# Kernel optimization log

Measured on AMD Instinct MI355X. Metric: run time of the kernel, lower is better.

## Reference

```python
import jax, jax.numpy as jnp
import numpy as np

VOCAB, D, SLOTS, K = 50257, 512, 16, 3
B, T_FULL = 64, 2049
EPS_LN = 1e-5


def setup_inputs() -> dict:
    key = jax.random.key(0)
    ks = jax.random.split(key, 12)
    u = jax.random.uniform(ks[0], (B, T_FULL - 1), jnp.float32)
    gumbel = -jnp.log(-jnp.log(u + 1e-8) + 1e-8)
    s = 0.02
    return {
        "seq": jax.random.randint(ks[1], (B, T_FULL), 0, VOCAB),
        "temperature": jnp.ones((), jnp.float32),
        "gumbel": gumbel,
        "embed": jax.random.normal(ks[2], (VOCAB, D), jnp.float32) * s,
        "W1": jax.random.normal(ks[3], (D, 2 * D), jnp.float32) * s,
        "b1": jnp.zeros((2 * D,), jnp.float32),
        "W2": jax.random.normal(ks[4], (2 * D, D), jnp.float32) * s,
        "b2": jnp.zeros((D,), jnp.float32),
        "gamma": jnp.ones((D,), jnp.float32),
        "beta": jnp.zeros((D,), jnp.float32),
        "Wg": jax.random.normal(ks[5], (D,), jnp.float32) * s,
        "bg": jnp.zeros((), jnp.float32),
        "Wr": jax.random.normal(ks[6], (D, D), jnp.float32) * s,
        "br": jnp.zeros((D,), jnp.float32),
        "Wo": jax.random.normal(ks[7], (D, VOCAB), jnp.float32) * s,
        "bo": jnp.zeros((VOCAB,), jnp.float32),
    }


def reference(seq, temperature, gumbel, embed, W1, b1, W2, b2, gamma, beta, Wg, bg, Wr, br, Wo, bo):
    # Encoder: embed -> FFN residual -> LayerNorm
    h = embed[seq]                                        # [B, T+1, D]
    ff = jnp.maximum(h @ W1 + b1, 0.0) @ W2 + b2
    x = h + ff
    mu = jnp.mean(x, -1, keepdims=True)
    var = jnp.mean((x - mu) ** 2, -1, keepdims=True)
    hiddens = (x - mu) * jax.lax.rsqrt(var + EPS_LN) * gamma + beta

    context = hiddens[:, :-1, :]                          # [B, T, D]
    gate = context @ Wg + bg                              # [B, T]

    # gumbel top-k with straight-through mask (forward value = hard mask)
    perturbed = (gate + gumbel) / temperature
    _, idx = jax.lax.top_k(perturbed, K)                  # [B, K]
    mask = jnp.zeros_like(gate).at[jnp.arange(B)[:, None], idx].set(1.0)
    soft = jax.nn.softmax(perturbed, axis=-1)
    sel = mask + soft - jax.lax.stop_gradient(soft)

    # gather selected hidden states, scatter_add into memory slots
    gw = jnp.take_along_axis(sel, idx, axis=1)            # [B, K]
    gh = jnp.take_along_axis(context, idx[..., None], axis=1)  # [B, K, D]
    weighted = gh * gw[..., None]
    slot_idx = jnp.arange(K) % SLOTS
    mem = jnp.zeros((B, SLOTS, D), hiddens.dtype).at[:, slot_idx, :].add(weighted)

    # attention read with last-position query
    q = hiddens[:, -1, :] @ Wr + br                       # [B, D]
    scores = jnp.einsum('bsd,bd->bs', mem, q)
    attn = jax.nn.softmax(scores, axis=-1)
    ctx = jnp.einsum('bs,bsd->bd', attn, mem)
    return ctx @ Wo + bo                                  # [B, vocab]
```

## Files before the change

kernel.cpp:

```cpp
#include <hip/hip_runtime.h>
#include <math.h>

#define TFULL 2049
#define TCTX  2048
#define Vm    50257

typedef __attribute__((ext_vector_type(8))) short bf16x8;
typedef __attribute__((ext_vector_type(4))) short s16x4;
typedef __attribute__((ext_vector_type(4))) float f32x4;

__device__ __forceinline__ float wred64(float v){
  #pragma unroll
  for (int m = 1; m < 64; m <<= 1) v += __shfl_xor(v, m, 64);
  return v;
}
__device__ __forceinline__ short bf16_rn(float x){
  union { float f; unsigned u; } c; c.f = x;
  unsigned r = c.u + 0x7fff + ((c.u >> 16) & 1);
  return (short)(r >> 16);
}
__device__ __forceinline__ float bf16_f(short s){
  union { float f; unsigned u; } c; c.u = ((unsigned)(unsigned short)s) << 16;
  return c.f;
}

#define FMA4(ACC_, S_, W_)                         \
  (ACC_).x = fmaf((S_), (W_).x, (ACC_).x);         \
  (ACC_).y = fmaf((S_), (W_).y, (ACC_).y);         \
  (ACC_).z = fmaf((S_), (W_).z, (ACC_).z);         \
  (ACC_).w = fmaf((S_), (W_).w, (ACC_).w);

__global__ void k0_setup(const float* __restrict__ gamma, const float* __restrict__ beta,
                         const float* __restrict__ Wg, float* __restrict__ scal){
  const int t = threadIdx.x;
  float wg = Wg[t];
  float g  = gamma[t]*wg, bw = beta[t]*wg;
  scal[2 + t] = g;
  g = wred64(g); bw = wred64(bw);
  __shared__ float ra[8], rb[8];
  if ((t & 63) == 0){ ra[t>>6] = g; rb[t>>6] = bw; }
  __syncthreads();
  if (t == 0){
    float G = 0.f, Bw = 0.f;
    #pragma unroll
    for (int i = 0; i < 8; ++i){ G += ra[i]; Bw += rb[i]; }
    scal[0] = G; scal[1] = Bw;
  }
}

__global__ __launch_bounds__(256) void kpack(const float* __restrict__ W, int N, int KB,
                                             short* __restrict__ hi, short* __restrict__ lo){
  int i = blockIdx.x*256 + threadIdx.x;
  if (i >= KB*N*4) return;
  int kq = i & 3;
  int n  = (i >> 2) % N;
  int kb = i / (N*4);
  const float* src = W + (kb*32 + kq*8)*N + n;
  bf16x8 h8, l8;
  #pragma unroll
  for (int j = 0; j < 8; ++j){
    float w = src[j*N];
    short h = bf16_rn(w);
    h8[j] = h;
    l8[j] = bf16_rn(w - bf16_f(h));
  }
  *(bf16x8*)(hi + i*8) = h8;
  *(bf16x8*)(lo + i*8) = l8;
}

__global__ __launch_bounds__(512, 2) void k1_main(
    const int*   __restrict__ seq,   const float* __restrict__ temp,
    const float* __restrict__ gumbel,const float* __restrict__ embed,
    const short* __restrict__ W1h,   const short* __restrict__ W1l,
    const float* __restrict__ b1,
    const short* __restrict__ W2h,   const short* __restrict__ W2l,
    const float* __restrict__ b2,
    const float* __restrict__ gamma, const float* __restrict__ beta,
    const float* __restrict__ bg,
    const float* __restrict__ scal,
    float* __restrict__ pert, float* __restrict__ qh)
{
  __shared__ short Ah[8*2048];
  __shared__ short Al[8*2048];
  __shared__ short Rbuf[32768];
  __shared__ float Xq[512];
  __shared__ int   srow[64];
  __shared__ float redS1[512], redS2[512], redSG[512];
  __shared__ float redMu[64], redRs[64];

  short* Rh = Rbuf;
  short* Rl = Rbuf + 16384;

  const int t    = threadIdx.x;
  const int tile = blockIdx.x;
  const int lane = t & 63;
  const int wv   = t >> 6;
  const int mrow = lane & 15;
  const int kq   = lane >> 4;
  const int crow0 = kq*4;

  if (t < 64) srow[t] = seq[tile*64 + t];
  __syncthreads();

  const f32x4* __restrict__ embv = (const f32x4*)embed;

  auto stageA = [&](int hh){
    #pragma unroll
    for (int k = 0; k < 8; ++k){
      int idx = k*512 + t;
      int tok = idx >> 6, c4 = idx & 63;
      f32x4 v = embv[srow[tok]*128 + hh*64 + c4];
      int dl = c4*4;
      int base = (dl>>5)*2048 + ((dl>>3)&3)*512 + tok*8 + (dl&7);
      short h0 = bf16_rn(v[0]), h1 = bf16_rn(v[1]), h2 = bf16_rn(v[2]), h3 = bf16_rn(v[3]);
      *(s16x4*)(Ah + base) = (s16x4){h0, h1, h2, h3};
      *(s16x4*)(Al + base) = (s16x4){ bf16_rn(v[0] - bf16_f(h0)),
                                      bf16_rn(v[1] - bf16_f(h1)),
                                      bf16_rn(v[2] - bf16_f(h2)),
                                      bf16_rn(v[3] - bf16_f(h3)) };
    }
  };

  f32x4 ff[4][4];
  #pragma unroll
  for (int i = 0; i < 4; ++i)
    #pragma unroll
    for (int j = 0; j < 4; ++j) ff[i][j] = (f32x4){0.f,0.f,0.f,0.f};

  const int aoff = kq*512 + mrow*8;
  int boff2[4];
  #pragma unroll
  for (int nt = 0; nt < 4; ++nt)
    boff2[nt] = (wv*64 + nt*16 + mrow)*32 + kq*8;

  #pragma unroll 1
  for (int ch = 0; ch < 4; ++ch){
    f32x4 acc[2][4];
    #pragma unroll
    for (int i = 0; i < 2; ++i)
      #pragma unroll
      for (int j = 0; j < 4; ++j) acc[i][j] = (f32x4){0.f,0.f,0.f,0.f};

    int boff1[2];
    #pragma unroll
    for (int nt = 0; nt < 2; ++nt)
      boff1[nt] = (ch*256 + wv*32 + nt*16 + mrow)*32 + kq*8;

    auto g1 = [&](int hh){
      const short* whB = W1h + hh*262144;
      const short* wlB = W1l + hh*262144;
      bf16x8 ah[2][4], al[2][4], bh[2][2], bl[2][2];
      #pragma unroll
      for (int mt = 0; mt < 4; ++mt){
        ah[0][mt] = *(const bf16x8*)(Ah + aoff + mt*128);
        al[0][mt] = *(const bf16x8*)(Al + aoff + mt*128);
      }
      #pragma unroll
      for (int nt = 0; nt < 2; ++nt){
        bh[0][nt] = *(const bf16x8*)(whB + boff1[nt]);
        bl[0][nt] = *(const bf16x8*)(wlB + boff1[nt]);
      }
      #pragma unroll
      for (int kbr = 0; kbr < 8; ++kbr){
        const int cur = kbr & 1, nxt = cur ^ 1;
        if (kbr < 7){
          #pragma unroll
          for (int mt = 0; mt < 4; ++mt){
            ah[nxt][mt] = *(const bf16x8*)(Ah + (kbr+1)*2048 + aoff + mt*128);
            al[nxt][mt] = *(const bf16x8*)(Al + (kbr+1)*2048 + aoff + mt*128);
          }
          #pragma unroll
          for (int nt = 0; nt < 2; ++nt){
            bh[nxt][nt] = *(const bf16x8*)(whB + (kbr+1)*32768 + boff1[nt]);
            bl[nxt][nt] = *(const bf16x8*)(wlB + (kbr+1)*32768 + boff1[nt]);
          }
        }
        #pragma unroll
        for (int nt = 0; nt < 2; ++nt)
          #pragma unroll
          for (int mt = 0; mt < 4; ++mt){
            acc[nt][mt] = __builtin_amdgcn_mfma_f32_16x16x32_bf16(ah[cur][mt], bh[cur][nt], acc[nt][mt], 0,0,0);
            acc[nt][mt] = __builtin_amdgcn_mfma_f32_16x16x32_bf16(al[cur][mt], bh[cur][nt], acc[nt][mt], 0,0,0);
            acc[nt][mt] = __builtin_amdgcn_mfma_f32_16x16x32_bf16(ah[cur][mt], bl[cur][nt], acc[nt][mt], 0,0,0);
          }
      }
    };

    stageA(0);
    __syncthreads();
    g1(0);
    __syncthreads();
    stageA(1);
    __syncthreads();
    g1(1);
    __syncthreads();

    #pragma unroll
    for (int nt = 0; nt < 2; ++nt){
      int jcol = wv*32 + nt*16 + mrow;
      float bb = b1[ch*256 + jcol];
      int rbase = (jcol>>5)*2048 + ((jcol>>3)&3)*512 + (jcol&7);
      #pragma unroll
      for (int mt = 0; mt < 4; ++mt){
        #pragma unroll
        for (int r = 0; r < 4; ++r){
          int tok = mt*16 + crow0 + r;
          float a = fmaxf(acc[nt][mt][r] + bb, 0.f);
          short h = bf16_rn(a);
          Rh[rbase + tok*8] = h;
          Rl[rbase + tok*8] = bf16_rn(a - bf16_f(h));
        }
      }
    }
    __syncthreads();

    {
      const short* w2hB = W2h + ch*131072;
      const short* w2lB = W2l + ch*131072;
      bf16x8 rh2[2][4], rl2[2][4], bh2[2][4], bl2[2][4];
      #pragma unroll
      for (int mt = 0; mt < 4; ++mt){
        rh2[0][mt] = *(const bf16x8*)(Rh + aoff + mt*128);
        rl2[0][mt] = *(const bf16x8*)(Rl + aoff + mt*128);
      }
      #pragma unroll
      for (int nt = 0; nt < 4; ++nt){
        bh2[0][nt] = *(const bf16x8*)(w2hB + boff2[nt]);
        bl2[0][nt] = *(const bf16x8*)(w2lB + boff2[nt]);
      }
      #pragma unroll
      for (int kb = 0; kb < 8; ++kb){
        const int cur = kb & 1, nxt = cur ^ 1;
        if (kb < 7){
          #pragma unroll
          for (int mt = 0; mt < 4; ++mt){
            rh2[nxt][mt] = *(const bf16x8*)(Rh + (kb+1)*2048 + aoff + mt*128);
            rl2[nxt][mt] = *(const bf16x8*)(Rl + (kb+1)*2048 + aoff + mt*128);
          }
          #pragma unroll
          for (int nt = 0; nt < 4; ++nt){
            bh2[nxt][nt] = *(const bf16x8*)(w2hB + (kb+1)*16384 + boff2[nt]);
            bl2[nxt][nt] = *(const bf16x8*)(w2lB + (kb+1)*16384 + boff2[nt]);
          }
        }
        #pragma unroll
        for (int nt = 0; nt < 4; ++nt)
          #pragma unroll
          for (int mt = 0; mt < 4; ++mt){
            ff[nt][mt] = __builtin_amdgcn_mfma_f32_16x16x32_bf16(rh2[cur][mt], bh2[cur][nt], ff[nt][mt], 0,0,0);
            ff[nt][mt] = __builtin_amdgcn_mfma_f32_16x16x32_bf16(rl2[cur][mt], bh2[cur][nt], ff[nt][mt], 0,0,0);
            ff[nt][mt] = __builtin_amdgcn_mfma_f32_16x16x32_bf16(rh2[cur][mt], bl2[cur][nt], ff[nt][mt], 0,0,0);
          }
      }
    }
  }

  __syncthreads();
  float* hbuf = (float*)Rbuf;
  #pragma unroll
  for (int k = 0; k < 8; ++k){
    int idx = k*512 + t;
    int tok = idx >> 6, c4 = idx & 63;
    f32x4 v = embv[srow[tok]*128 + c4];
    f32x4 hv;
    #pragma unroll
    for (int j = 0; j < 4; ++j){
      short hi = bf16_rn(v[j]);
      hv[j] = bf16_f(hi) + bf16_f(bf16_rn(v[j] - bf16_f(hi)));
    }
    *(f32x4*)(hbuf + tok*256 + c4*4) = hv;
  }
  __syncthreads();

  const float G1 = scal[0], BW = scal[1];
  const float* gWg = scal + 2;
  const float bgv  = bg[0];
  const float invT = 1.0f / temp[0];
  int rem  = (tile*64) % 2049;
  int qtok = 2048 - rem;

  float ps1[4][4], ps2[4][4], psg[4][4];
  #pragma unroll
  for (int mt = 0; mt < 4; ++mt)
    #pragma unroll
    for (int r = 0; r < 4; ++r){ ps1[mt][r]=0.f; ps2[mt][r]=0.f; psg[mt][r]=0.f; }

  #pragma unroll
  for (int nt = 0; nt < 4; ++nt){
    int d = wv*64 + nt*16 + mrow;
    float b2v = b2[d];
    float gw  = gWg[d];
    if (wv >= 4){
      int abase = ((d - 256)>>5)*2048 + ((d>>3)&3)*512 + (d&7);
      #pragma unroll
      for (int mt = 0; mt < 4; ++mt){
        #pragma unroll
        for (int r = 0; r < 4; ++r){
          int tok = mt*16 + crow0 + r;
          float h = bf16_f(Ah[abase + tok*8]) + bf16_f(Al[abase + tok*8]);
          float x = h + ff[nt][mt][r] + b2v;
          ps1[mt][r] += x;
          ps2[mt][r] = fmaf(x, x, ps2[mt][r]);
          psg[mt][r] = fmaf(x, gw, psg[mt][r]);
          if (tok == qtok) Xq[d] = x;
        }
      }
    } else {
      #pragma unroll
      for (int mt = 0; mt < 4; ++mt){
        #pragma unroll
        for (int r = 0; r < 4; ++r){
          int tok = mt*16 + crow0 + r;
          float h = hbuf[tok*256 + d];
          float x = h + ff[nt][mt][r] + b2v;
          ps1[mt][r] += x;
          ps2[mt][r] = fmaf(x, x, ps2[mt][r]);
          psg[mt][r] = fmaf(x, gw, psg[mt][r]);
          if (tok == qtok) Xq[d] = x;
        }
      }
    }
  }
  #pragma unroll
  for (int mt = 0; mt < 4; ++mt){
    #pragma unroll
    for (int r = 0; r < 4; ++r){
      float a = ps1[mt][r], b = ps2[mt][r], c = psg[mt][r];
      #pragma unroll
      for (int m = 1; m < 16; m <<= 1){
        a += __shfl_xor(a, m, 64);
        b += __shfl_xor(b, m, 64);
        c += __shfl_xor(c, m, 64);
      }
      if (mrow == 0){
        int tok = mt*16 + crow0 + r;
        redS1[tok*8 + wv] = a;
        redS2[tok*8 + wv] = b;
        redSG[tok*8 + wv] = c;
      }
    }
  }
  __syncthreads();

  if (t < 64){
    float S1 = 0.f, S2 = 0.f, SG = 0.f;
    #pragma unroll
    for (int w = 0; w < 8; ++w){
      S1 += redS1[t*8 + w];
      S2 += redS2[t*8 + w];
      SG += redSG[t*8 + w];
    }
    float mu  = S1 * (1.f/512.f);
    float var = S2 * (1.f/512.f) - mu*mu;
    float rs  = rsqrtf(var + 1e-5f);
    redMu[t] = mu; redRs[t] = rs;
    int id  = tile*64 + t;
    int b   = id / 2049;
    int pos = id - b*2049;
    if (pos < TCTX){
      float gate = rs*(SG - mu*G1) + BW + bgv;
      float pv = (gate + __builtin_nontemporal_load(gumbel + b*TCTX + pos)) * invT;
      __builtin_nontemporal_store(pv, pert + b*TCTX + pos);
    }
  }
  __syncthreads();

  if (qtok < 64 && t < 256){
    int id = tile*64 + qtok;
    int b  = id / 2049;
    float mu = redMu[qtok], rs = redRs[qtok];
    int d = t*2;
    qh[b*512 + d]     = (Xq[d]  -mu)*rs*gamma[d]   + beta[d];
    qh[b*512 + d + 1] = (Xq[d+1]-mu)*rs*gamma[d+1] + beta[d+1];
  }
}

__global__ __launch_bounds__(256) void k2_topk(const float* __restrict__ pert,
                                               int* __restrict__ idxw){
  __shared__ float v[2048];
  __shared__ float wvv[256];
  __shared__ int   wii[256];
  const int b = blockIdx.x, t = threadIdx.x;
  for (int i = t; i < 2048; i += 256) v[i] = pert[b*TCTX + i];
  __syncthreads();
  for (int r = 0; r < 3; ++r){
    float best = -INFINITY; int bi = 1<<30;
    for (int i = t; i < 2048; i += 256){
      float x = v[i];
      if (x > best || (x == best && i < bi)){ best = x; bi = i; }
    }
    wvv[t] = best; wii[t] = bi;
    __syncthreads();
    for (int s = 128; s > 0; s >>= 1){
      if (t < s){
        float ov = wvv[t+s]; int oi = wii[t+s];
        if (ov > wvv[t] || (ov == wvv[t] && oi < wii[t])){ wvv[t] = ov; wii[t] = oi; }
      }
      __syncthreads();
    }
    if (t == 0){ idxw[b*3 + r] = wii[0]; v[wii[0]] = -INFINITY; }
    __syncthreads();
  }
}

__global__ __launch_bounds__(256) void k3_rows(const int* __restrict__ seq,
    const float* __restrict__ embed, const float* __restrict__ W1, const float* __restrict__ b1,
    const float* __restrict__ W2,    const float* __restrict__ b2,
    const float* __restrict__ gamma, const float* __restrict__ beta,
    const int* __restrict__ idxw, float* __restrict__ memr)
{
  __shared__ float hs[512];
  __shared__ float rbuf[1024];
  __shared__ float red1[4], red2[4];
  const int t   = threadIdx.x;
  const int blk = blockIdx.x;
  const int b = blk / 3, kk = blk - b*3;
  const int pos = idxw[b*3 + kk];
  const int row = seq[b*TFULL + pos];
  ((float2*)hs)[t] = ((const float2*)(embed + row*512))[t];
  __syncthreads();
  const float4* W1v = (const float4*)W1;
  float4 a = make_float4(0,0,0,0);
  #pragma unroll 4
  for (int d = 0; d < 512; ++d){
    float xb = hs[d];
    float4 wq = W1v[d*256 + t];
    FMA4(a, xb, wq);
  }
  float4 bq = ((const float4*)b1)[t];
  float4 r;
  r.x = fmaxf(a.x+bq.x, 0.f); r.y = fmaxf(a.y+bq.y, 0.f);
  r.z = fmaxf(a.z+bq.z, 0.f); r.w = fmaxf(a.w+bq.w, 0.f);
  ((float4*)rbuf)[t] = r;
  __syncthreads();
  const float2* W2v2 = (const float2*)W2;
  float fx = 0.f, fy = 0.f;
  #pragma unroll 4
  for (int j = 0; j < 1024; ++j){
    float rb = rbuf[j];
    float2 wq = W2v2[j*256 + t];
    fx = fmaf(rb, wq.x, fx); fy = fmaf(rb, wq.y, fy);
  }
  float2 b2q = ((const float2*)b2)[t];
  float2 hx  = ((float2*)hs)[t];
  float x0 = hx.x + fx + b2q.x;
  float x1 = hx.y + fy + b2q.y;
  float s1 = wred64(x0 + x1);
  float s2 = wred64(x0*x0 + x1*x1);
  if ((t & 63) == 0){ red1[t>>6] = s1; red2[t>>6] = s2; }
  __syncthreads();
  float S1 = red1[0]+red1[1]+red1[2]+red1[3];
  float S2 = red2[0]+red2[1]+red2[2]+red2[3];
  float mu  = S1*(1.f/512.f);
  float var = S2*(1.f/512.f) - mu*mu;
  float rs  = rsqrtf(var + 1e-5f);
  const int dd = t*2;
  memr[(b*3+kk)*512 + dd]     = (x0-mu)*rs*gamma[dd]   + beta[dd];
  memr[(b*3+kk)*512 + dd + 1] = (x1-mu)*rs*gamma[dd+1] + beta[dd+1];
}

__global__ __launch_bounds__(256) void k4_attn(const float* __restrict__ qh,
    const float* __restrict__ Wr, const float* __restrict__ br,
    const float* __restrict__ memr, float* __restrict__ ctxT)
{
  __shared__ float hq[512];
  __shared__ float red[12];
  const int t = threadIdx.x, b = blockIdx.x;
  ((float2*)hq)[t] = ((const float2*)(qh + b*512))[t];
  __syncthreads();
  const float2* Wrv = (const float2*)Wr;
  float qx = 0.f, qy = 0.f;
  #pragma unroll 4
  for (int d = 0; d < 512; ++d){
    float hb = hq[d];
    float2 wq = Wrv[d*256 + t];
    qx = fmaf(hb, wq.x, qx); qy = fmaf(hb, wq.y, qy);
  }
  float2 brq = ((const float2*)br)[t];
  qx += brq.x; qy += brq.y;
  const int dd = t*2;
  const float* m0 = memr + (b*3+0)*512;
  const float* m1 = memr + (b*3+1)*512;
  const float* m2 = memr + (b*3+2)*512;
  float p0 = wred64(qx*m0[dd] + qy*m0[dd+1]);
  float p1 = wred64(qx*m1[dd] + qy*m1[dd+1]);
  float p2 = wred64(qx*m2[dd] + qy*m2[dd+1]);
  if ((t & 63) == 0){ int w = t>>6; red[w*3+0]=p0; red[w*3+1]=p1; red[w*3+2]=p2; }
  __syncthreads();
  float s0 = red[0]+red[3]+red[6]+red[9];
  float s1 = red[1]+red[4]+red[7]+red[10];
  float s2 = red[2]+red[5]+red[8]+red[11];
  float m  = fmaxf(fmaxf(s0, s1), fmaxf(s2, 0.f));
  float e0 = expf(s0-m), e1 = expf(s1-m), e2 = expf(s2-m);
  float den = e0 + e1 + e2 + 13.f*expf(-m);
  float a0 = e0/den, a1 = e1/den, a2 = e2/den;
  float c0 = a0*m0[dd]   + a1*m1[dd]   + a2*m2[dd];
  float c1 = a0*m0[dd+1] + a1*m1[dd+1] + a2*m2[dd+1];
  ctxT[dd*64 + b]     = c0;
  ctxT[(dd+1)*64 + b] = c1;
}

__global__ __launch_bounds__(256) void k5_out(const float* __restrict__ ctxT,
    const float* __restrict__ Wo, const float* __restrict__ bo,
    float* __restrict__ out)
{
  const int v  = blockIdx.x*256 + threadIdx.x;
  const int vc = v < Vm ? v : Vm-1;
  float acc[64];
  #pragma unroll
  for (int b = 0; b < 64; ++b) acc[b] = 0.f;
  for (int d = 0; d < 512; ++d){
    float w = Wo[d*Vm + vc];
    const float* c = ctxT + d*64;
    #pragma unroll
    for (int b = 0; b < 64; ++b) acc[b] = fmaf(c[b], w, acc[b]);
  }
  if (v < Vm){
    float bb = bo[v];
    #pragma unroll
    for (int b = 0; b < 64; ++b) out[b*Vm + v] = acc[b] + bb;
  }
}

extern "C" void kernel_launch(void* const* d_in, const int* in_sizes, int n_in,
                              void* d_out, int out_size, void* d_ws, size_t ws_size,
                              hipStream_t stream){
  (void)in_sizes; (void)n_in; (void)out_size; (void)ws_size;
  const int*   seq   = (const int*)d_in[0];
  const float* temp  = (const float*)d_in[1];
  const float* gum   = (const float*)d_in[2];
  const float* embed = (const float*)d_in[3];
  const float* W1    = (const float*)d_in[4];
  const float* b1    = (const float*)d_in[5];
  const float* W2    = (const float*)d_in[6];
  const float* b2    = (const float*)d_in[7];
  const float* gamma = (const float*)d_in[8];
  const float* beta  = (const float*)d_in[9];
  const float* Wg    = (const float*)d_in[10];
  const float* bg    = (const float*)d_in[11];
  const float* Wr    = (const float*)d_in[12];
  const float* br    = (const float*)d_in[13];
  const float* Wo    = (const float*)d_in[14];
  const float* bo    = (const float*)d_in[15];
  float* out = (float*)d_out;

  float* wsf  = (float*)d_ws;
  float* pert = wsf;
  float* qh   = wsf + 131072;
  float* memr = wsf + 163840;
  float* ctxT = wsf + 262144;
  float* scal = wsf + 294912;
  int*   idxw = (int*)(wsf + 295936);
  short* W1h  = (short*)(wsf + 296192);
  short* W1l  = W1h + 512*1024;
  short* W2h  = W1l + 512*1024;
  short* W2l  = W2h + 1024*512;

  k0_setup<<<1, 512, 0, stream>>>(gamma, beta, Wg, scal);
  kpack<<<256, 256, 0, stream>>>(W1, 1024, 16, W1h, W1l);
  kpack<<<256, 256, 0, stream>>>(W2, 512, 32, W2h, W2l);
  k1_main<<<2049, 512, 0, stream>>>(seq, temp, gum, embed, W1h, W1l, b1,
                                    W2h, W2l, b2, gamma, beta, bg, scal, pert, qh);
  k2_topk<<<64, 256, 0, stream>>>(pert, idxw);
  k3_rows<<<192, 256, 0, stream>>>(seq, embed, W1, b1, W2, b2, gamma, beta, idxw, memr);
  k4_attn<<<64, 256, 0, stream>>>(qh, Wr, br, memr, ctxT);
  k5_out<<<197, 256, 0, stream>>>(ctxT, Wo, bo, out);
}
```

Measured before the change: 2.145 ms.

## Halve k1 token tile to 32, pad LDS layout, raise occupancy, batch k3 rows

The main encoder kernel now processes 32 tokens per block instead of 64, doubling the grid. It also drops the register double-buffering of MFMA operands and raises launch bounds to 4 blocks per CU, so more waves can hide latency. LDS planes are padded (stride 264/1056) to reduce bank conflicts. k3 now computes all three selected rows in one block so each W1/W2 weight load is shared across them. The trade-off is that each W1/W2 tile is fetched by twice as many blocks, giving less weight reuse per block.

```diff
diff --git a/kernel.cpp b/kernel.cpp
--- a/kernel.cpp
+++ b/kernel.cpp
@@ -4,6 +4,9 @@
 #define TFULL 2049
 #define TCTX  2048
 #define Vm    50257
+
+#define PLN 264
+#define KBP 1056
 
 typedef __attribute__((ext_vector_type(8))) short bf16x8;
 typedef __attribute__((ext_vector_type(4))) short s16x4;
@@ -68,7 +71,7 @@
   *(bf16x8*)(lo + i*8) = l8;
 }
 
-__global__ __launch_bounds__(512, 2) void k1_main(
+__global__ __launch_bounds__(512, 4) void k1_main(
     const int*   __restrict__ seq,   const float* __restrict__ temp,
     const float* __restrict__ gumbel,const float* __restrict__ embed,
     const short* __restrict__ W1h,   const short* __restrict__ W1l,
@@ -80,16 +83,16 @@
     const float* __restrict__ scal,
     float* __restrict__ pert, float* __restrict__ qh)
 {
-  __shared__ short Ah[8*2048];
-  __shared__ short Al[8*2048];
-  __shared__ short Rbuf[32768];
+  __shared__ __align__(16) short Ah[8*KBP];
+  __shared__ __align__(16) short Al[8*KBP];
+  __shared__ __align__(16) short Rbuf[2*8*KBP];
   __shared__ float Xq[512];
-  __shared__ int   srow[64];
-  __shared__ float redS1[512], redS2[512], redSG[512];
-  __shared__ float redMu[64], redRs[64];
+  __shared__ int   srow[32];
+  __shared__ float redS1[256], redS2[256], redSG[256];
+  __shared__ float redMu[32], redRs[32];
 
   short* Rh = Rbuf;
-  short* Rl = Rbuf + 16384;
+  short* Rl = Rbuf + 8*KBP;
 
   const int t    = threadIdx.x;
   const int tile = blockIdx.x;
@@ -99,19 +102,19 @@
   const int kq   = lane >> 4;
   const int crow0 = kq*4;
 
-  if (t < 64) srow[t] = seq[tile*64 + t];
+  if (t < 32) srow[t] = seq[tile*32 + t];
   __syncthreads();
 
   const f32x4* __restrict__ embv = (const f32x4*)embed;
 
   auto stageA = [&](int hh){
     #pragma unroll
-    for (int k = 0; k < 8; ++k){
+    for (int k = 0; k < 4; ++k){
       int idx = k*512 + t;
       int tok = idx >> 6, c4 = idx & 63;
       f32x4 v = embv[srow[tok]*128 + hh*64 + c4];
       int dl = c4*4;
-      int base = (dl>>5)*2048 + ((dl>>3)&3)*512 + tok*8 + (dl&7);
+      int base = (dl>>5)*KBP + ((dl>>3)&3)*PLN + tok*8 + (dl&7);
       short h0 = bf16_rn(v[0]), h1 = bf16_rn(v[1]), h2 = bf16_rn(v[2]), h3 = bf16_rn(v[3]);
       *(s16x4*)(Ah + base) = (s16x4){h0, h1, h2, h3};
       *(s16x4*)(Al + base) = (s16x4){ bf16_rn(v[0] - bf16_f(h0)),
@@ -121,13 +124,13 @@
     }
   };
 
-  f32x4 ff[4][4];
+  f32x4 ff[4][2];
   #pragma unroll
   for (int i = 0; i < 4; ++i)
     #pragma unroll
-    for (int j = 0; j < 4; ++j) ff[i][j] = (f32x4){0.f,0.f,0.f,0.f};
-
-  const int aoff = kq*512 + mrow*8;
+    for (int j = 0; j < 2; ++j) ff[i][j] = (f32x4){0.f,0.f,0.f,0.f};
+
+  const int aoff = kq*PLN + mrow*8;
   int boff2[4];
   #pragma unroll
   for (int nt = 0; nt < 4; ++nt)
@@ -135,11 +138,11 @@
 
   #pragma unroll 1
   for (int ch = 0; ch < 4; ++ch){
-    f32x4 acc[2][4];
+    f32x4 acc[2][2];
     #pragma unroll
     for (int i = 0; i < 2; ++i)
       #pragma unroll
-      for (int j = 0; j < 4; ++j) acc[i][j] = (f32x4){0.f,0.f,0.f,0.f};
+      for (int j = 0; j < 2; ++j) acc[i][j] = (f32x4){0.f,0.f,0.f,0.f};
 
     int boff1[2];
     #pragma unroll
@@ -149,40 +152,23 @@
     auto g1 = [&](int hh){
       const short* whB = W1h + hh*262144;
       const short* wlB = W1l + hh*262144;
-      bf16x8 ah[2][4], al[2][4], bh[2][2], bl[2][2];
-      #pragma unroll
-      for (int mt = 0; mt < 4; ++mt){
-        ah[0][mt] = *(const bf16x8*)(Ah + aoff + mt*128);
-        al[0][mt] = *(const bf16x8*)(Al + aoff + mt*128);
-      }
-      #pragma unroll
-      for (int nt = 0; nt < 2; ++nt){
-        bh[0][nt] = *(const bf16x8*)(whB + boff1[nt]);
-        bl[0][nt] = *(const bf16x8*)(wlB + boff1[nt]);
-      }
       #pragma unroll
       for (int kbr = 0; kbr < 8; ++kbr){
-        const int cur = kbr & 1, nxt = cur ^ 1;
-        if (kbr < 7){
-          #pragma unroll
-          for (int mt = 0; mt < 4; ++mt){
-            ah[nxt][mt] = *(const bf16x8*)(Ah + (kbr+1)*2048 + aoff + mt*128);
-            al[nxt][mt] = *(const bf16x8*)(Al + (kbr+1)*2048 + aoff + mt*128);
-          }
-          #pragma unroll
-          for (int nt = 0; nt < 2; ++nt){
-            bh[nxt][nt] = *(const bf16x8*)(whB + (kbr+1)*32768 + boff1[nt]);
-            bl[nxt][nt] = *(const bf16x8*)(wlB + (kbr+1)*32768 + boff1[nt]);
-          }
+        bf16x8 ah0 = *(const bf16x8*)(Ah + kbr*KBP + aoff);
+        bf16x8 al0 = *(const bf16x8*)(Al + kbr*KBP + aoff);
+        bf16x8 ah1 = *(const bf16x8*)(Ah + kbr*KBP + aoff + 128);
+        bf16x8 al1 = *(const bf16x8*)(Al + kbr*KBP + aoff + 128);
+        #pragma unroll
+        for (int nt = 0; nt < 2; ++nt){
+          bf16x8 bh = *(const bf16x8*)(whB + kbr*32768 + boff1[nt]);
+          bf16x8 bl = *(const bf16x8*)(wlB + kbr*32768 + boff1[nt]);
+          acc[nt][0] = __builtin_amdgcn_mfma_f32_16x16x32_bf16(ah0, bh, acc[nt][0], 0,0,0);
+          acc[nt][0] = __builtin_amdgcn_mfma_f32_16x16x32_bf16(al0, bh, acc[nt][0], 0,0,0);
+          acc[nt][0] = __builtin_amdgcn_mfma_f32_16x16x32_bf16(ah0, bl, acc[nt][0], 0,0,0);
+          acc[nt][1] = __builtin_amdgcn_mfma_f32_16x16x32_bf16(ah1, bh, acc[nt][1], 0,0,0);
+          acc[nt][1] = __builtin_amdgcn_mfma_f32_16x16x32_bf16(al1, bh, acc[nt][1], 0,0,0);
+          acc[nt][1] = __builtin_amdgcn_mfma_f32_16x16x32_bf16(ah1, bl, acc[nt][1], 0,0,0);
         }
-        #pragma unroll
-        for (int nt = 0; nt < 2; ++nt)
-          #pragma unroll
-          for (int mt = 0; mt < 4; ++mt){
-            acc[nt][mt] = __builtin_amdgcn_mfma_f32_16x16x32_bf16(ah[cur][mt], bh[cur][nt], acc[nt][mt], 0,0,0);
-            acc[nt][mt] = __builtin_amdgcn_mfma_f32_16x16x32_bf16(al[cur][mt], bh[cur][nt], acc[nt][mt], 0,0,0);
-            acc[nt][mt] = __builtin_amdgcn_mfma_f32_16x16x32_bf16(ah[cur][mt], bl[cur][nt], acc[nt][mt], 0,0,0);
-          }
       }
     };
 
@@ -199,9 +185,9 @@
     for (int nt = 0; nt < 2; ++nt){
       int jcol = wv*32 + nt*16 + mrow;
       float bb = b1[ch*256 + jcol];
-      int rbase = (jcol>>5)*2048 + ((jcol>>3)&3)*512 + (jcol&7);
-      #pragma unroll
-      for (int mt = 0; mt < 4; ++mt){
+      int rbase = (jcol>>5)*KBP + ((jcol>>3)&3)*PLN + (jcol&7);
+      #pragma unroll
+      for (int mt = 0; mt < 2; ++mt){
         #pragma unroll
         for (int r = 0; r < 4; ++r){
           int tok = mt*16 + crow0 + r;
@@ -217,40 +203,23 @@
     {
       const short* w2hB = W2h + ch*131072;
       const short* w2lB = W2l + ch*131072;
-      bf16x8 rh2[2][4], rl2[2][4], bh2[2][4], bl2[2][4];
-      #pragma unroll
-      for (int mt = 0; mt < 4; ++mt){
-        rh2[0][mt] = *(const bf16x8*)(Rh + aoff + mt*128);
-        rl2[0][mt] = *(const bf16x8*)(Rl + aoff + mt*128);
-      }
-      #pragma unroll
-      for (int nt = 0; nt < 4; ++nt){
-        bh2[0][nt] = *(const bf16x8*)(w2hB + boff2[nt]);
-        bl2[0][nt] = *(const bf16x8*)(w2lB + boff2[nt]);
-      }
       #pragma unroll
       for (int kb = 0; kb < 8; ++kb){
-        const int cur = kb & 1, nxt = cur ^ 1;
-        if (kb < 7){
-          #pragma unroll
-          for (int mt = 0; mt < 4; ++mt){
-            rh2[nxt][mt] = *(const bf16x8*)(Rh + (kb+1)*2048 + aoff + mt*128);
-            rl2[nxt][mt] = *(const bf16x8*)(Rl + (kb+1)*2048 + aoff + mt*128);
-          }
-          #pragma unroll
-          for (int nt = 0; nt < 4; ++nt){
-            bh2[nxt][nt] = *(const bf16x8*)(w2hB + (kb+1)*16384 + boff2[nt]);
-            bl2[nxt][nt] = *(const bf16x8*)(w2lB + (kb+1)*16384 + boff2[nt]);
-          }
+        bf16x8 rh0 = *(const bf16x8*)(Rh + kb*KBP + aoff);
+        bf16x8 rl0 = *(const bf16x8*)(Rl + kb*KBP + aoff);
+        bf16x8 rh1 = *(const bf16x8*)(Rh + kb*KBP + aoff + 128);
+        bf16x8 rl1 = *(const bf16x8*)(Rl + kb*KBP + aoff + 128);
+        #pragma unroll
+        for (int nt = 0; nt < 4; ++nt){
+          bf16x8 bh = *(const bf16x8*)(w2hB + kb*16384 + boff2[nt]);
+          bf16x8 bl = *(const bf16x8*)(w2lB + kb*16384 + boff2[nt]);
+          ff[nt][0] = __builtin_amdgcn_mfma_f32_16x16x32_bf16(rh0, bh, ff[nt][0], 0,0,0);
+          ff[nt][0] = __builtin_amdgcn_mfma_f32_16x16x32_bf16(rl0, bh, ff[nt][0], 0,0,0);
+          ff[nt][0] = __builtin_amdgcn_mfma_f32_16x16x32_bf16(rh0, bl, ff[nt][0], 0,0,0);
+          ff[nt][1] = __builtin_amdgcn_mfma_f32_16x16x32_bf16(rh1, bh, ff[nt][1], 0,0,0);
+          ff[nt][1] = __builtin_amdgcn_mfma_f32_16x16x32_bf16(rl1, bh, ff[nt][1], 0,0,0);
+          ff[nt][1] = __builtin_amdgcn_mfma_f32_16x16x32_bf16(rh1, bl, ff[nt][1], 0,0,0);
         }
-        #pragma unroll
-        for (int nt = 0; nt < 4; ++nt)
-          #pragma unroll
-          for (int mt = 0; mt < 4; ++mt){
-            ff[nt][mt] = __builtin_amdgcn_mfma_f32_16x16x32_bf16(rh2[cur][mt], bh2[cur][nt], ff[nt][mt], 0,0,0);
-            ff[nt][mt] = __builtin_amdgcn_mfma_f32_16x16x32_bf16(rl2[cur][mt], bh2[cur][nt], ff[nt][mt], 0,0,0);
-            ff[nt][mt] = __builtin_amdgcn_mfma_f32_16x16x32_bf16(rh2[cur][mt], bl2[cur][nt], ff[nt][mt], 0,0,0);
-          }
       }
     }
   }
@@ -258,7 +227,7 @@
   __syncthreads();
   float* hbuf = (float*)Rbuf;
   #pragma unroll
-  for (int k = 0; k < 8; ++k){
+  for (int k = 0; k < 4; ++k){
     int idx = k*512 + t;
     int tok = idx >> 6, c4 = idx & 63;
     f32x4 v = embv[srow[tok]*128 + c4];
@@ -276,12 +245,12 @@
   const float* gWg = scal + 2;
   const float bgv  = bg[0];
   const float invT = 1.0f / temp[0];
-  int rem  = (tile*64) % 2049;
+  int rem  = (tile*32) % 2049;
   int qtok = 2048 - rem;
 
-  float ps1[4][4], ps2[4][4], psg[4][4];
-  #pragma unroll
-  for (int mt = 0; mt < 4; ++mt)
+  float ps1[2][4], ps2[2][4], psg[2][4];
+  #pragma unroll
+  for (int mt = 0; mt < 2; ++mt)
     #pragma unroll
     for (int r = 0; r < 4; ++r){ ps1[mt][r]=0.f; ps2[mt][r]=0.f; psg[mt][r]=0.f; }
 
@@ -291,9 +260,9 @@
     float b2v = b2[d];
     float gw  = gWg[d];
     if (wv >= 4){
-      int abase = ((d - 256)>>5)*2048 + ((d>>3)&3)*512 + (d&7);
-      #pragma unroll
-      for (int mt = 0; mt < 4; ++mt){
+      int abase = ((d - 256)>>5)*KBP + ((d>>3)&3)*PLN + (d&7);
+      #pragma unroll
+      for (int mt = 0; mt < 2; ++mt){
         #pragma unroll
         for (int r = 0; r < 4; ++r){
           int tok = mt*16 + crow0 + r;
@@ -307,7 +276,7 @@
       }
     } else {
       #pragma unroll
-      for (int mt = 0; mt < 4; ++mt){
+      for (int mt = 0; mt < 2; ++mt){
         #pragma unroll
         for (int r = 0; r < 4; ++r){
           int tok = mt*16 + crow0 + r;
@@ -322,7 +291,7 @@
     }
   }
   #pragma unroll
-  for (int mt = 0; mt < 4; ++mt){
+  for (int mt = 0; mt < 2; ++mt){
     #pragma unroll
     for (int r = 0; r < 4; ++r){
       float a = ps1[mt][r], b = ps2[mt][r], c = psg[mt][r];
@@ -342,7 +311,7 @@
   }
   __syncthreads();
 
-  if (t < 64){
+  if (t < 32){
     float S1 = 0.f, S2 = 0.f, SG = 0.f;
     #pragma unroll
     for (int w = 0; w < 8; ++w){
@@ -354,7 +323,7 @@
     float var = S2 * (1.f/512.f) - mu*mu;
     float rs  = rsqrtf(var + 1e-5f);
     redMu[t] = mu; redRs[t] = rs;
-    int id  = tile*64 + t;
+    int id  = tile*32 + t;
     int b   = id / 2049;
     int pos = id - b*2049;
     if (pos < TCTX){
@@ -365,8 +334,8 @@
   }
   __syncthreads();
 
-  if (qtok < 64 && t < 256){
-    int id = tile*64 + qtok;
+  if (qtok < 32 && t < 256){
+    int id = tile*32 + qtok;
     int b  = id / 2049;
     float mu = redMu[qtok], rs = redRs[qtok];
     int d = t*2;
@@ -409,54 +378,79 @@
     const float* __restrict__ gamma, const float* __restrict__ beta,
     const int* __restrict__ idxw, float* __restrict__ memr)
 {
-  __shared__ float hs[512];
-  __shared__ float rbuf[1024];
-  __shared__ float red1[4], red2[4];
-  const int t   = threadIdx.x;
-  const int blk = blockIdx.x;
-  const int b = blk / 3, kk = blk - b*3;
-  const int pos = idxw[b*3 + kk];
-  const int row = seq[b*TFULL + pos];
-  ((float2*)hs)[t] = ((const float2*)(embed + row*512))[t];
+  __shared__ float hs[3*512];
+  __shared__ float rbuf[3*1024];
+  __shared__ float red1[12], red2[12];
+  const int t  = threadIdx.x;
+  const int b  = blockIdx.x;
+  const int wv = t >> 6;
+  #pragma unroll
+  for (int kk = 0; kk < 3; ++kk){
+    int pos = idxw[b*3 + kk];
+    int row = seq[b*TFULL + pos];
+    ((float2*)(hs + kk*512))[t] = ((const float2*)(embed + row*512))[t];
+  }
   __syncthreads();
   const float4* W1v = (const float4*)W1;
-  float4 a = make_float4(0,0,0,0);
-  #pragma unroll 4
+  float4 a0 = make_float4(0,0,0,0), a1 = a0, a2 = a0;
+  #pragma unroll 2
   for (int d = 0; d < 512; ++d){
-    float xb = hs[d];
     float4 wq = W1v[d*256 + t];
-    FMA4(a, xb, wq);
+    float h0 = hs[d], h1 = hs[512+d], h2 = hs[1024+d];
+    FMA4(a0, h0, wq); FMA4(a1, h1, wq); FMA4(a2, h2, wq);
   }
   float4 bq = ((const float4*)b1)[t];
-  float4 r;
-  r.x = fmaxf(a.x+bq.x, 0.f); r.y = fmaxf(a.y+bq.y, 0.f);
-  r.z = fmaxf(a.z+bq.z, 0.f); r.w = fmaxf(a.w+bq.w, 0.f);
-  ((float4*)rbuf)[t] = r;
+  float4 r0, r1, r2;
+  r0.x = fmaxf(a0.x+bq.x,0.f); r0.y = fmaxf(a0.y+bq.y,0.f);
+  r0.z = fmaxf(a0.z+bq.z,0.f); r0.w = fmaxf(a0.w+bq.w,0.f);
+  r1.x = fmaxf(a1.x+bq.x,0.f); r1.y = fmaxf(a1.y+bq.y,0.f);
+  r1.z = fmaxf(a1.z+bq.z,0.f); r1.w = fmaxf(a1.w+bq.w,0.f);
+  r2.x = fmaxf(a2.x+bq.x,0.f); r2.y = fmaxf(a2.y+bq.y,0.f);
+  r2.z = fmaxf(a2.z+bq.z,0.f); r2.w = fmaxf(a2.w+bq.w,0.f);
+  ((float4*)rbuf)[t]          = r0;
+  ((float4*)(rbuf+1024))[t]   = r1;
+  ((float4*)(rbuf+2048))[t]   = r2;
   __syncthreads();
   const float2* W2v2 = (const float2*)W2;
-  float fx = 0.f, fy = 0.f;
-  #pragma unroll 4
+  float f0x=0.f,f0y=0.f,f1x=0.f,f1y=0.f,f2x=0.f,f2y=0.f;
+  #pragma unroll 2
   for (int j = 0; j < 1024; ++j){
-    float rb = rbuf[j];
     float2 wq = W2v2[j*256 + t];
-    fx = fmaf(rb, wq.x, fx); fy = fmaf(rb, wq.y, fy);
+    float q0 = rbuf[j], q1 = rbuf[1024+j], q2 = rbuf[2048+j];
+    f0x = fmaf(q0, wq.x, f0x); f0y = fmaf(q0, wq.y, f0y);
+    f1x = fmaf(q1, wq.x, f1x); f1y = fmaf(q1, wq.y, f1y);
+    f2x = fmaf(q2, wq.x, f2x); f2y = fmaf(q2, wq.y, f2y);
   }
   float2 b2q = ((const float2*)b2)[t];
-  float2 hx  = ((float2*)hs)[t];
-  float x0 = hx.x + fx + b2q.x;
-  float x1 = hx.y + fy + b2q.y;
-  float s1 = wred64(x0 + x1);
-  float s2 = wred64(x0*x0 + x1*x1);
-  if ((t & 63) == 0){ red1[t>>6] = s1; red2[t>>6] = s2; }
-  __syncthreads();
-  float S1 = red1[0]+red1[1]+red1[2]+red1[3];
-  float S2 = red2[0]+red2[1]+red2[2]+red2[3];
-  float mu  = S1*(1.f/512.f);
-  float var = S2*(1.f/512.f) - mu*mu;
-  float rs  = rsqrtf(var + 1e-5f);
   const int dd = t*2;
-  memr[(b*3+kk)*512 + dd]     = (x0-mu)*rs*gamma[dd]   + beta[dd];
-  memr[(b*3+kk)*512 + dd + 1] = (x1-mu)*rs*gamma[dd+1] + beta[dd+1];
+  float2 hx0 = ((float2*)hs)[t];
+  float2 hx1 = ((float2*)(hs+512))[t];
+  float2 hx2 = ((float2*)(hs+1024))[t];
+  float x00 = hx0.x + f0x + b2q.x, x01 = hx0.y + f0y + b2q.y;
+  float x10 = hx1.x + f1x + b2q.x, x11 = hx1.y + f1y + b2q.y;
+  float x20 = hx2.x + f2x + b2q.x, x21 = hx2.y + f2y + b2q.y;
+  float s10 = wred64(x00 + x01), s20 = wred64(x00*x00 + x01*x01);
+  float s11 = wred64(x10 + x11), s21 = wred64(x10*x10 + x11*x11);
+  float s12 = wred64(x20 + x21), s22 = wred64(x20*x20 + x21*x21);
+  if ((t & 63) == 0){
+    red1[0*4+wv] = s10; red2[0*4+wv] = s20;
+    red1[1*4+wv] = s11; red2[1*4+wv] = s21;
+    red1[2*4+wv] = s12; red2[2*4+wv] = s22;
+  }
+  __syncthreads();
+  float gx = gamma[dd], gy = gamma[dd+1], bx = beta[dd], by = beta[dd+1];
+  #pragma unroll
+  for (int kk = 0; kk < 3; ++kk){
+    float S1 = red1[kk*4+0]+red1[kk*4+1]+red1[kk*4+2]+red1[kk*4+3];
+    float S2 = red2[kk*4+0]+red2[kk*4+1]+red2[kk*4+2]+red2[kk*4+3];
+    float mu  = S1*(1.f/512.f);
+    float var = S2*(1.f/512.f) - mu*mu;
+    float rs  = rsqrtf(var + 1e-5f);
+    float x0 = (kk==0) ? x00 : (kk==1) ? x10 : x20;
+    float x1 = (kk==0) ? x01 : (kk==1) ? x11 : x21;
+    memr[(b*3+kk)*512 + dd]     = (x0-mu)*rs*gx + bx;
+    memr[(b*3+kk)*512 + dd + 1] = (x1-mu)*rs*gy + by;
+  }
 }
 
 __global__ __launch_bounds__(256) void k4_attn(const float* __restrict__ qh,
@@ -559,10 +553,10 @@
   k0_setup<<<1, 512, 0, stream>>>(gamma, beta, Wg, scal);
   kpack<<<256, 256, 0, stream>>>(W1, 1024, 16, W1h, W1l);
   kpack<<<256, 256, 0, stream>>>(W2, 512, 32, W2h, W2l);
-  k1_main<<<2049, 512, 0, stream>>>(seq, temp, gum, embed, W1h, W1l, b1,
+  k1_main<<<4098, 512, 0, stream>>>(seq, temp, gum, embed, W1h, W1l, b1,
                                     W2h, W2l, b2, gamma, beta, bg, scal, pert, qh);
   k2_topk<<<64, 256, 0, stream>>>(pert, idxw);
-  k3_rows<<<192, 256, 0, stream>>>(seq, embed, W1, b1, W2, b2, gamma, beta, idxw, memr);
+  k3_rows<<<64, 256, 0, stream>>>(seq, embed, W1, b1, W2, b2, gamma, beta, idxw, memr);
   k4_attn<<<64, 256, 0, stream>>>(qh, Wr, br, memr, ctxT);
   k5_out<<<197, 256, 0, stream>>>(ctxT, Wo, bo, out);
 }
```

Measured after the change: 2.141 ms. About the same (-0.2%).
